# Optimization experiments

Measured on AMD Instinct MI355X. Metric: run time of the kernel, lower is better.

Reference implementation:

```python
import jax, jax.numpy as jnp
import numpy as np

B, I, O, H = 16384, 32, 64, 64  # batch, inp_dim, out_dim (towers), hidden width


def setup_inputs() -> dict:
    key = jax.random.key(0)
    ks = jax.random.split(key, 5)
    s0 = 1.0 / np.sqrt(I)
    sh = 1.0 / np.sqrt(H)
    return {
        "x": jax.random.normal(ks[0], (B, I), dtype=jnp.float32),
        "W0": jax.random.normal(ks[1], (O, I, H), dtype=jnp.float32) * s0,
        "b0": jnp.zeros((O, H), dtype=jnp.float32),
        "W1": jax.random.normal(ks[2], (O, H, H), dtype=jnp.float32) * sh,
        "b1": jnp.zeros((O, H), dtype=jnp.float32),
        "W2": jax.random.normal(ks[3], (O, H, H), dtype=jnp.float32) * sh,
        "b2": jnp.zeros((O, H), dtype=jnp.float32),
        "W3": jax.random.normal(ks[4], (O, H), dtype=jnp.float32) * sh,
        "b3": jnp.zeros((O,), dtype=jnp.float32),
    }


def reference(x, W0, b0, W1, b1, W2, b2, W3, b3):
    # O independent towers: Dense(H,relu) x3 then Dense(1); concat along axis=1.
    # Expressed as batched einsums over the tower axis 'o' (same math as the loop).
    h = jax.nn.relu(jnp.einsum('bi,oih->boh', x, W0) + b0)   # [B,O,H]
    h = jax.nn.relu(jnp.einsum('boh,ohk->bok', h, W1) + b1)  # [B,O,H]
    h = jax.nn.relu(jnp.einsum('boh,ohk->bok', h, W2) + b2)  # [B,O,H]
    out = jnp.einsum('boh,oh->bo', h, W3) + b3               # [B,O]
    return out
```

## Files before the change

### kernel.cpp

```cpp
#include <hip/hip_runtime.h>


typedef float  f32x4 __attribute__((ext_vector_type(4)));
typedef _Float16 h8  __attribute__((ext_vector_type(8)));
typedef unsigned int uint4v __attribute__((ext_vector_type(4)));

static constexpr int Bsz  = 16384;
static constexpr int Idim = 32;
static constexpr int Odim = 64;
static constexpr int BPT  = 8;
static constexpr int ROWTILES = (Bsz / 64) / BPT;

static constexpr int IMG = 21504;

#define GLD16(gp, lp) __builtin_amdgcn_global_load_lds( \
    (const __attribute__((address_space(1))) void*)(gp), \
    (__attribute__((address_space(3))) void*)(lp), 16, 0, 0)

__device__ __forceinline__ unsigned short f2h(float f) {
    _Float16 h = (_Float16)f;
    return __builtin_bit_cast(unsigned short, h);
}

__device__ __forceinline__ unsigned cvt_relu_pk(float lo, float hi) {
    unsigned v = __builtin_bit_cast(unsigned, __builtin_amdgcn_cvt_pkrtz(lo, hi));
    unsigned r;
    asm("v_pk_max_f16 %0, %1, 0" : "=v"(r) : "v"(v));
    return r;
}

__device__ __forceinline__ unsigned cvt_pk2(float lo, float hi) {
    return __builtin_bit_cast(unsigned, __builtin_amdgcn_cvt_pkrtz(lo, hi));
}

__device__ __forceinline__ int pi_slot(int in) {
    return 32 * (in >> 5) + 8 * ((in >> 2) & 3) + 4 * ((in >> 4) & 1) + (in & 3);
}

__global__ __launch_bounds__(256) void prep_kernel(
    const float* __restrict__ W0, const float* __restrict__ b0,
    const float* __restrict__ W1, const float* __restrict__ b1,
    const float* __restrict__ W2, const float* __restrict__ b2,
    const float* __restrict__ W3, char* __restrict__ ws)
{
    const int o = blockIdx.x >> 2, q = blockIdx.x & 3, tid = threadIdx.x;
    char* img = ws + o * IMG;
    unsigned short* Wt0 = (unsigned short*)img;
    unsigned short* Wt1 = (unsigned short*)(img + 4096);
    unsigned short* Wt2 = (unsigned short*)(img + 12288);
    unsigned short* w3s = (unsigned short*)(img + 20480);
    float*          bsf = (float*)(img + 20608);

    {
        int f = q * 256 + tid;
        f32x4 v1 = *(const f32x4*)&W1[o * 4096 + f * 4];
        f32x4 v2 = *(const f32x4*)&W2[o * 4096 + f * 4];
        int in = (f * 4) >> 6;
        int h0 = (f * 4) & 63;
        int S  = pi_slot(in);
#pragma unroll
        for (int j = 0; j < 4; ++j) {
            int h = h0 + j;
            int cw = S ^ ((((h >> 2) ^ h) & 7) << 3);
            Wt1[h * 64 + cw] = f2h(v1[j]);
            Wt2[h * 64 + cw] = f2h(v2[j]);
        }
    }
    if (q < 2) {
        int f = q * 256 + tid;
        f32x4 v = *(const f32x4*)&W0[o * 2048 + f * 4];
        int i  = (f * 4) >> 6;
        int h0 = (f * 4) & 63;
#pragma unroll
        for (int j = 0; j < 4; ++j) {
            int h = h0 + j;
            Wt0[h * 32 + (i ^ ((((h >> 2) ^ h) & 3) << 3))] = f2h(v[j]);
        }
    }
    if (q == 3 && tid < 64) {
        w3s[pi_slot(tid)] = f2h(W3[o * 64 + tid]);
        bsf[tid]       = b0[o * 64 + tid];
        bsf[64 + tid]  = b1[o * 64 + tid];
        bsf[128 + tid] = b2[o * 64 + tid];
    }
}

__global__ __launch_bounds__(256, 2) void towers_kernel(
    const float* __restrict__ x, const char* __restrict__ ws,
    const float* __restrict__ b3, float* __restrict__ out)
{
    __shared__ __align__(16) char SH[IMG];

    const int tid  = threadIdx.x;
    const int o    = blockIdx.x / BPT;
    const int slot = blockIdx.x % BPT;
    const int l = tid & 63, w = tid >> 6;
    const int c = l & 15,  g = l >> 4;

    const float* xbase = x + (slot * ROWTILES * 64 + w * 16 + c) * Idim + g * 8;
    f32x4 nxa0 = *(const f32x4*)(xbase);
    f32x4 nxb0 = *(const f32x4*)(xbase + 4);
    f32x4 nxa1 = *(const f32x4*)(xbase + 2048);
    f32x4 nxb1 = *(const f32x4*)(xbase + 2052);

    {
        const char* img = ws + o * IMG;
#pragma unroll
        for (int ch = 0; ch < 6; ++ch) {
            int k = ch * 4 + w;
            if (k < 21)
                GLD16(img + k * 1024 + l * 16, SH + k * 1024);
        }
    }
    __syncthreads();

    const unsigned short* Wt0 = (const unsigned short*)SH;
    const unsigned short* Wt1 = (const unsigned short*)(SH + 4096);
    const unsigned short* w3s = (const unsigned short*)(SH + 20480);
    const float*          bsf = (const float*)(SH + 20608);

    h8 wf0[4], wf1f[4][2];
#pragma unroll
    for (int n = 0; n < 4; ++n) {
        int h = n * 16 + c;
        wf0[n] = *(const h8*)&Wt0[h * 32 + ((g * 8) ^ ((((h >> 2) ^ h) & 3) << 3))];
        int key = ((h >> 2) ^ h) & 7;
#pragma unroll
        for (int s = 0; s < 2; ++s)
            wf1f[n][s] = *(const h8*)&Wt1[h * 64 + ((s * 32 + g * 8) ^ (key << 3))];
    }
    h8 w3a[2];
    w3a[0] = *(const h8*)&w3s[g * 8];
    w3a[1] = *(const h8*)&w3s[32 + g * 8];

    int off2[4][2];
#pragma unroll
    for (int n = 0; n < 4; ++n) {
        int h = n * 16 + c;
        int key = ((h >> 2) ^ h) & 7;
#pragma unroll
        for (int s = 0; s < 2; ++s)
            off2[n][s] = 12288 + 2 * (h * 64 + ((s * 32 + g * 8) ^ (key << 3)));
    }

    f32x4 b0f[4], b1f[4], b2f[4];
#pragma unroll
    for (int n = 0; n < 4; ++n) {
        b0f[n] = *(const f32x4*)&bsf[      n * 16 + g * 4];
        b1f[n] = *(const f32x4*)&bsf[ 64 + n * 16 + g * 4];
        b2f[n] = *(const f32x4*)&bsf[128 + n * 16 + g * 4];
    }
    f32x4 c3 = {0.f, 0.f, 0.f, 0.f};
    if (g == 0) c3[0] = b3[o];

    float* obase = out + (slot * ROWTILES * 64 + w * 16 + c) * Odim + o;

    for (int tt = 0; tt < ROWTILES; tt += 2) {
        f32x4 xa0 = nxa0, xb0 = nxb0, xa1 = nxa1, xb1 = nxb1;
        if (tt + 2 < ROWTILES) {
            const float* np = xbase + (tt + 2) * 2048;
            nxa0 = *(const f32x4*)(np);
            nxb0 = *(const f32x4*)(np + 4);
            nxa1 = *(const f32x4*)(np + 2048);
            nxb1 = *(const f32x4*)(np + 2052);
        }

        uint4v xd0, xd1;
        xd0.x = cvt_pk2(xa0[0], xa0[1]); xd0.y = cvt_pk2(xa0[2], xa0[3]);
        xd0.z = cvt_pk2(xb0[0], xb0[1]); xd0.w = cvt_pk2(xb0[2], xb0[3]);
        xd1.x = cvt_pk2(xa1[0], xa1[1]); xd1.y = cvt_pk2(xa1[2], xa1[3]);
        xd1.z = cvt_pk2(xb1[0], xb1[1]); xd1.w = cvt_pk2(xb1[2], xb1[3]);
        h8 a0_0 = __builtin_bit_cast(h8, xd0);
        h8 a0_1 = __builtin_bit_cast(h8, xd1);

        f32x4 acc0[4], acc1[4];
#pragma unroll
        for (int n = 0; n < 4; ++n) {
            acc0[n] = __builtin_amdgcn_mfma_f32_16x16x32_f16(wf0[n], a0_0, b0f[n], 0, 0, 0);
            acc1[n] = __builtin_amdgcn_mfma_f32_16x16x32_f16(wf0[n], a0_1, b0f[n], 0, 0, 0);
        }

        unsigned p0[4][2], p1[4][2];
#pragma unroll
        for (int n = 0; n < 4; ++n) {
            p0[n][0] = cvt_relu_pk(acc0[n][0], acc0[n][1]);
            p0[n][1] = cvt_relu_pk(acc0[n][2], acc0[n][3]);
            p1[n][0] = cvt_relu_pk(acc1[n][0], acc1[n][1]);
            p1[n][1] = cvt_relu_pk(acc1[n][2], acc1[n][3]);
        }
        h8 Blo0 = __builtin_bit_cast(h8, uint4v{p0[0][0], p0[0][1], p0[1][0], p0[1][1]});
        h8 Bhi0 = __builtin_bit_cast(h8, uint4v{p0[2][0], p0[2][1], p0[3][0], p0[3][1]});
        h8 Blo1 = __builtin_bit_cast(h8, uint4v{p1[0][0], p1[0][1], p1[1][0], p1[1][1]});
        h8 Bhi1 = __builtin_bit_cast(h8, uint4v{p1[2][0], p1[2][1], p1[3][0], p1[3][1]});

#pragma unroll
        for (int n = 0; n < 4; ++n) {
            acc0[n] = __builtin_amdgcn_mfma_f32_16x16x32_f16(wf1f[n][0], Blo0, b1f[n], 0, 0, 0);
            acc1[n] = __builtin_amdgcn_mfma_f32_16x16x32_f16(wf1f[n][0], Blo1, b1f[n], 0, 0, 0);
            acc0[n] = __builtin_amdgcn_mfma_f32_16x16x32_f16(wf1f[n][1], Bhi0, acc0[n], 0, 0, 0);
            acc1[n] = __builtin_amdgcn_mfma_f32_16x16x32_f16(wf1f[n][1], Bhi1, acc1[n], 0, 0, 0);
        }
#pragma unroll
        for (int n = 0; n < 4; ++n) {
            p0[n][0] = cvt_relu_pk(acc0[n][0], acc0[n][1]);
            p0[n][1] = cvt_relu_pk(acc0[n][2], acc0[n][3]);
            p1[n][0] = cvt_relu_pk(acc1[n][0], acc1[n][1]);
            p1[n][1] = cvt_relu_pk(acc1[n][2], acc1[n][3]);
        }
        Blo0 = __builtin_bit_cast(h8, uint4v{p0[0][0], p0[0][1], p0[1][0], p0[1][1]});
        Bhi0 = __builtin_bit_cast(h8, uint4v{p0[2][0], p0[2][1], p0[3][0], p0[3][1]});
        Blo1 = __builtin_bit_cast(h8, uint4v{p1[0][0], p1[0][1], p1[1][0], p1[1][1]});
        Bhi1 = __builtin_bit_cast(h8, uint4v{p1[2][0], p1[2][1], p1[3][0], p1[3][1]});

        {
            const char* base = (const char*)SH;
            h8 w2[4];
#pragma unroll
            for (int n = 0; n < 4; ++n) {
                int a = off2[n][0];
                asm("" : "+v"(a));
                w2[n] = *(const h8*)(base + a);
            }
#pragma unroll
            for (int n = 0; n < 4; ++n) {
                acc0[n] = __builtin_amdgcn_mfma_f32_16x16x32_f16(w2[n], Blo0, b2f[n], 0, 0, 0);
                acc1[n] = __builtin_amdgcn_mfma_f32_16x16x32_f16(w2[n], Blo1, b2f[n], 0, 0, 0);
            }
#pragma unroll
            for (int n = 0; n < 4; ++n) {
                int a = off2[n][1];
                asm("" : "+v"(a));
                w2[n] = *(const h8*)(base + a);
            }
#pragma unroll
            for (int n = 0; n < 4; ++n) {
                acc0[n] = __builtin_amdgcn_mfma_f32_16x16x32_f16(w2[n], Bhi0, acc0[n], 0, 0, 0);
                acc1[n] = __builtin_amdgcn_mfma_f32_16x16x32_f16(w2[n], Bhi1, acc1[n], 0, 0, 0);
            }
        }
#pragma unroll
        for (int n = 0; n < 4; ++n) {
            p0[n][0] = cvt_relu_pk(acc0[n][0], acc0[n][1]);
            p0[n][1] = cvt_relu_pk(acc0[n][2], acc0[n][3]);
            p1[n][0] = cvt_relu_pk(acc1[n][0], acc1[n][1]);
            p1[n][1] = cvt_relu_pk(acc1[n][2], acc1[n][3]);
        }
        Blo0 = __builtin_bit_cast(h8, uint4v{p0[0][0], p0[0][1], p0[1][0], p0[1][1]});
        Bhi0 = __builtin_bit_cast(h8, uint4v{p0[2][0], p0[2][1], p0[3][0], p0[3][1]});
        Blo1 = __builtin_bit_cast(h8, uint4v{p1[0][0], p1[0][1], p1[1][0], p1[1][1]});
        Bhi1 = __builtin_bit_cast(h8, uint4v{p1[2][0], p1[2][1], p1[3][0], p1[3][1]});

        f32x4 acc3_0, acc3_1;
        acc3_0 = __builtin_amdgcn_mfma_f32_16x16x32_f16(w3a[0], Blo0, c3,     0, 0, 0);
        acc3_1 = __builtin_amdgcn_mfma_f32_16x16x32_f16(w3a[0], Blo1, c3,     0, 0, 0);
        acc3_0 = __builtin_amdgcn_mfma_f32_16x16x32_f16(w3a[1], Bhi0, acc3_0, 0, 0, 0);
        acc3_1 = __builtin_amdgcn_mfma_f32_16x16x32_f16(w3a[1], Bhi1, acc3_1, 0, 0, 0);

        if (g == 0) {
            obase[(tt)     * 64 * Odim] = acc3_0[0];
            obase[(tt + 1) * 64 * Odim] = acc3_1[0];
        }
    }
}

extern "C" void kernel_launch(void* const* d_in, const int* in_sizes, int n_in,
                              void* d_out, int out_size, void* d_ws, size_t ws_size,
                              hipStream_t stream) {
    const float* x  = (const float*)d_in[0];
    const float* W0 = (const float*)d_in[1];
    const float* b0 = (const float*)d_in[2];
    const float* W1 = (const float*)d_in[3];
    const float* b1 = (const float*)d_in[4];
    const float* W2 = (const float*)d_in[5];
    const float* b2 = (const float*)d_in[6];
    const float* W3 = (const float*)d_in[7];
    const float* b3 = (const float*)d_in[8];
    float* out = (float*)d_out;
    char* ws = (char*)d_ws;

    prep_kernel<<<dim3(Odim * 4), dim3(256), 0, stream>>>(W0, b0, W1, b1, W2, b2, W3, ws);
    towers_kernel<<<dim3(Odim * BPT), dim3(256), 0, stream>>>(x, ws, b3, out);
}
```

Measured before the change: 33.00 us.

## Pre-convert x to fp16 in prep, double blocks per tower, add MFMA priority

The prep kernel gains 512 extra blocks that convert x to fp16 once into the workspace. The towers kernel then loads half-width x instead of converting fp32 on every tower. BPT doubles to 16, occupancy hint rises to 3 blocks per SM, and s_setprio wraps the MFMA sections to favour matrix issue. This cuts the repeated x traffic and conversion across the 64 towers, at the cost of an extra workspace write/read and a longer prep kernel.

After: 44.09 us. 1.34x slower.

```diff
diff --git a/kernel.cpp b/kernel.cpp
--- a/kernel.cpp
+++ b/kernel.cpp
@@ -3,15 +3,17 @@
 
 typedef float  f32x4 __attribute__((ext_vector_type(4)));
 typedef _Float16 h8  __attribute__((ext_vector_type(8)));
+typedef unsigned int uint2v __attribute__((ext_vector_type(2)));
 typedef unsigned int uint4v __attribute__((ext_vector_type(4)));
 
 static constexpr int Bsz  = 16384;
 static constexpr int Idim = 32;
 static constexpr int Odim = 64;
-static constexpr int BPT  = 8;
+static constexpr int BPT  = 16;
 static constexpr int ROWTILES = (Bsz / 64) / BPT;
 
 static constexpr int IMG = 21504;
+static constexpr int XH_OFF = 64 * IMG;
 
 #define GLD16(gp, lp) __builtin_amdgcn_global_load_lds( \
     (const __attribute__((address_space(1))) void*)(gp), \
@@ -29,21 +31,28 @@
     return r;
 }
 
-__device__ __forceinline__ unsigned cvt_pk2(float lo, float hi) {
-    return __builtin_bit_cast(unsigned, __builtin_amdgcn_cvt_pkrtz(lo, hi));
-}
-
 __device__ __forceinline__ int pi_slot(int in) {
     return 32 * (in >> 5) + 8 * ((in >> 2) & 3) + 4 * ((in >> 4) & 1) + (in & 3);
 }
 
 __global__ __launch_bounds__(256) void prep_kernel(
+    const float* __restrict__ x,
     const float* __restrict__ W0, const float* __restrict__ b0,
     const float* __restrict__ W1, const float* __restrict__ b1,
     const float* __restrict__ W2, const float* __restrict__ b2,
     const float* __restrict__ W3, char* __restrict__ ws)
 {
-    const int o = blockIdx.x >> 2, q = blockIdx.x & 3, tid = threadIdx.x;
+    const int tid = threadIdx.x;
+    if (blockIdx.x >= 256) {
+        int idx = (blockIdx.x - 256) * 256 + tid;
+        f32x4 v = *(const f32x4*)&x[idx * 4];
+        uint2v d;
+        d.x = (unsigned)f2h(v[0]) | ((unsigned)f2h(v[1]) << 16);
+        d.y = (unsigned)f2h(v[2]) | ((unsigned)f2h(v[3]) << 16);
+        *(uint2v*)(ws + XH_OFF + idx * 8) = d;
+        return;
+    }
+    const int o = blockIdx.x >> 2, q = blockIdx.x & 3;
     char* img = ws + o * IMG;
     unsigned short* Wt0 = (unsigned short*)img;
     unsigned short* Wt1 = (unsigned short*)(img + 4096);
@@ -85,9 +94,9 @@
     }
 }
 
-__global__ __launch_bounds__(256, 2) void towers_kernel(
-    const float* __restrict__ x, const char* __restrict__ ws,
-    const float* __restrict__ b3, float* __restrict__ out)
+__global__ __launch_bounds__(256, 3) void towers_kernel(
+    const char* __restrict__ ws, const float* __restrict__ b3,
+    float* __restrict__ out)
 {
     __shared__ __align__(16) char SH[IMG];
 
@@ -97,11 +106,10 @@
     const int l = tid & 63, w = tid >> 6;
     const int c = l & 15,  g = l >> 4;
 
-    const float* xbase = x + (slot * ROWTILES * 64 + w * 16 + c) * Idim + g * 8;
-    f32x4 nxa0 = *(const f32x4*)(xbase);
-    f32x4 nxb0 = *(const f32x4*)(xbase + 4);
-    f32x4 nxa1 = *(const f32x4*)(xbase + 2048);
-    f32x4 nxb1 = *(const f32x4*)(xbase + 2052);
+    const _Float16* xh = (const _Float16*)(ws + XH_OFF);
+    const _Float16* xbase = xh + (slot * ROWTILES * 64 + w * 16 + c) * Idim + g * 8;
+    h8 nx0 = *(const h8*)(xbase);
+    h8 nx1 = *(const h8*)(xbase + 2048);
 
     {
         const char* img = ws + o * IMG;
@@ -156,29 +164,20 @@
     float* obase = out + (slot * ROWTILES * 64 + w * 16 + c) * Odim + o;
 
     for (int tt = 0; tt < ROWTILES; tt += 2) {
-        f32x4 xa0 = nxa0, xb0 = nxb0, xa1 = nxa1, xb1 = nxb1;
+        h8 x0 = nx0, x1 = nx1;
         if (tt + 2 < ROWTILES) {
-            const float* np = xbase + (tt + 2) * 2048;
-            nxa0 = *(const f32x4*)(np);
-            nxb0 = *(const f32x4*)(np + 4);
-            nxa1 = *(const f32x4*)(np + 2048);
-            nxb1 = *(const f32x4*)(np + 2052);
-        }
-
-        uint4v xd0, xd1;
-        xd0.x = cvt_pk2(xa0[0], xa0[1]); xd0.y = cvt_pk2(xa0[2], xa0[3]);
-        xd0.z = cvt_pk2(xb0[0], xb0[1]); xd0.w = cvt_pk2(xb0[2], xb0[3]);
-        xd1.x = cvt_pk2(xa1[0], xa1[1]); xd1.y = cvt_pk2(xa1[2], xa1[3]);
-        xd1.z = cvt_pk2(xb1[0], xb1[1]); xd1.w = cvt_pk2(xb1[2], xb1[3]);
-        h8 a0_0 = __builtin_bit_cast(h8, xd0);
-        h8 a0_1 = __builtin_bit_cast(h8, xd1);
+            nx0 = *(const h8*)(xbase + (tt + 2) * 2048);
+            nx1 = *(const h8*)(xbase + (tt + 3) * 2048);
+        }
 
         f32x4 acc0[4], acc1[4];
-#pragma unroll
-        for (int n = 0; n < 4; ++n) {
-            acc0[n] = __builtin_amdgcn_mfma_f32_16x16x32_f16(wf0[n], a0_0, b0f[n], 0, 0, 0);
-            acc1[n] = __builtin_amdgcn_mfma_f32_16x16x32_f16(wf0[n], a0_1, b0f[n], 0, 0, 0);
-        }
+        __builtin_amdgcn_s_setprio(1);
+#pragma unroll
+        for (int n = 0; n < 4; ++n) {
+            acc0[n] = __builtin_amdgcn_mfma_f32_16x16x32_f16(wf0[n], x0, b0f[n], 0, 0, 0);
+            acc1[n] = __builtin_amdgcn_mfma_f32_16x16x32_f16(wf0[n], x1, b0f[n], 0, 0, 0);
+        }
+        __builtin_amdgcn_s_setprio(0);
 
         unsigned p0[4][2], p1[4][2];
 #pragma unroll
@@ -193,6 +192,7 @@
         h8 Blo1 = __builtin_bit_cast(h8, uint4v{p1[0][0], p1[0][1], p1[1][0], p1[1][1]});
         h8 Bhi1 = __builtin_bit_cast(h8, uint4v{p1[2][0], p1[2][1], p1[3][0], p1[3][1]});
 
+        __builtin_amdgcn_s_setprio(1);
 #pragma unroll
         for (int n = 0; n < 4; ++n) {
             acc0[n] = __builtin_amdgcn_mfma_f32_16x16x32_f16(wf1f[n][0], Blo0, b1f[n], 0, 0, 0);
@@ -200,6 +200,7 @@
             acc0[n] = __builtin_amdgcn_mfma_f32_16x16x32_f16(wf1f[n][1], Bhi0, acc0[n], 0, 0, 0);
             acc1[n] = __builtin_amdgcn_mfma_f32_16x16x32_f16(wf1f[n][1], Bhi1, acc1[n], 0, 0, 0);
         }
+        __builtin_amdgcn_s_setprio(0);
 #pragma unroll
         for (int n = 0; n < 4; ++n) {
             p0[n][0] = cvt_relu_pk(acc0[n][0], acc0[n][1]);
@@ -250,11 +251,13 @@
         Blo1 = __builtin_bit_cast(h8, uint4v{p1[0][0], p1[0][1], p1[1][0], p1[1][1]});
         Bhi1 = __builtin_bit_cast(h8, uint4v{p1[2][0], p1[2][1], p1[3][0], p1[3][1]});
 
+        __builtin_amdgcn_s_setprio(1);
         f32x4 acc3_0, acc3_1;
         acc3_0 = __builtin_amdgcn_mfma_f32_16x16x32_f16(w3a[0], Blo0, c3,     0, 0, 0);
         acc3_1 = __builtin_amdgcn_mfma_f32_16x16x32_f16(w3a[0], Blo1, c3,     0, 0, 0);
         acc3_0 = __builtin_amdgcn_mfma_f32_16x16x32_f16(w3a[1], Bhi0, acc3_0, 0, 0, 0);
         acc3_1 = __builtin_amdgcn_mfma_f32_16x16x32_f16(w3a[1], Bhi1, acc3_1, 0, 0, 0);
+        __builtin_amdgcn_s_setprio(0);
 
         if (g == 0) {
             obase[(tt)     * 64 * Odim] = acc3_0[0];
@@ -278,6 +281,6 @@
     float* out = (float*)d_out;
     char* ws = (char*)d_ws;
 
-    prep_kernel<<<dim3(Odim * 4), dim3(256), 0, stream>>>(W0, b0, W1, b1, W2, b2, W3, ws);
-    towers_kernel<<<dim3(Odim * BPT), dim3(256), 0, stream>>>(x, ws, b3, out);
-}
+    prep_kernel<<<dim3(256 + 512), dim3(256), 0, stream>>>(x, W0, b0, W1, b1, W2, b2, W3, ws);
+    towers_kernel<<<dim3(Odim * BPT), dim3(256), 0, stream>>>(ws, b3, out);
+}
```
